# Optimization experiments

Measured on AMD Instinct MI355X. Metric: run time of the kernel, lower is better.

Reference implementation:

```python
import jax, jax.numpy as jnp
import numpy as np

BN_EPS = 1e-5


def _get_normals(radius, nsample, xyz):
    # xyz: [B, N, 3] -> normals [B, N, 3] (eigenvector of smallest eigenvalue)
    B, N, _ = xyz.shape
    sq = jnp.sum(xyz * xyz, axis=-1)                      # [B, N]
    sqrdists = sq[:, :, None] + sq[:, None, :] - 2.0 * jnp.einsum('bnc,bmc->bnm', xyz, xyz)
    ar = jnp.arange(N, dtype=jnp.int32)
    group_idx = jnp.where(sqrdists > radius * radius, N, ar[None, None, :])  # [B, N, N]
    group_idx = jnp.sort(group_idx, axis=-1)[:, :, :nsample]                 # [B, N, ns]
    group_idx = jnp.where(group_idx == N, group_idx[:, :, :1], group_idx)
    group_points = jax.vmap(lambda pts, idx: pts[idx])(xyz, group_idx)       # [B, N, ns, 3]
    centered = group_points - group_points.mean(axis=2, keepdims=True)
    cov = jnp.einsum('bnsc,bnsd->bncd', centered, centered)                  # [B, N, 3, 3]
    _, eigen_vectors = jnp.linalg.eigh(cov)
    return eigen_vectors[..., 0]


def _conv_bn(h, w, b, g, be, m, v, relu=True):
    # h: [B, N, Cin]; 1x1 Conv1d == per-point linear; BN in eval mode
    h = h @ w.T + b
    h = (h - m) / jnp.sqrt(v + BN_EPS) * g + be
    return jax.nn.relu(h) if relu else h


def setup_inputs() -> dict:
    key = jax.random.key(0)
    ks = jax.random.split(key, 32)
    B, N = 4, 4096
    inp = {
        'x': jax.random.uniform(ks[0], (B, N, 3), dtype=jnp.float32),
        'small': 0.2,
        'large': 0.3,
    }
    chans = [(1, 16), (16, 32), (32, 16), (16, 1)]
    for li, (cin, cout) in enumerate(chans, start=1):
        k = 4 * li
        inp[f'w{li}'] = jax.random.normal(ks[k], (cout, cin), dtype=jnp.float32) * (1.0 / np.sqrt(cin))
        inp[f'b{li}'] = jax.random.normal(ks[k + 1], (cout,), dtype=jnp.float32) * 0.1
        inp[f'g{li}'] = jax.random.uniform(ks[k + 2], (cout,), dtype=jnp.float32) + 0.5
        inp[f'be{li}'] = jax.random.normal(ks[k + 3], (cout,), dtype=jnp.float32) * 0.1
        inp[f'm{li}'] = jnp.zeros((cout,), dtype=jnp.float32)
        inp[f'v{li}'] = jnp.ones((cout,), dtype=jnp.float32)
    return inp


def reference(x, small, large,
              w1, b1, g1, be1, m1, v1,
              w2, b2, g2, be2, m2, v2,
              w3, b3, g3, be3, m3, v3,
              w4, b4, g4, be4, m4, v4):
    xyz = x[:, :, :3]
    small_n = _get_normals(small, 32, xyz)   # [B, N, 3]
    large_n = _get_normals(large, 64, xyz)
    curvature = jnp.linalg.norm((small_n - large_n) * 0.5, axis=2)  # [B, N]
    h = curvature[..., None]                                        # [B, N, 1]
    h = _conv_bn(h, w1, b1, g1, be1, m1, v1)
    h = _conv_bn(h, w2, b2, g2, be2, m2, v2)
    h = _conv_bn(h, w3, b3, g3, be3, m3, v3)
    h = _conv_bn(h, w4, b4, g4, be4, m4, v4, relu=False)
    return h[..., 0]                                                # [B, N]
```

## Files before the change

### kernel.cpp

```cpp
#include <hip/hip_runtime.h>
#include <math.h>

#define BLAS_FMA 1
#define SYR2_VARIANT 0

#define DEV static __device__ __forceinline__

DEV float fA(float a, float b){ return __fadd_rn(a,b); }
DEV float fSb(float a, float b){ return __fsub_rn(a,b); }
DEV float fM(float a, float b){ return __fmul_rn(a,b); }
DEV float fDv(float a, float b){ return __fdiv_rn(a,b); }
DEV float fQ(float a){ return __fsqrt_rn(a); }
DEV float fF(float a, float b, float c){ return __builtin_fmaf(a,b,c); }
DEV float fSGN(float a, float b){ return copysignf(a,b); }

DEV float slapy2f(float x, float y){
  float xa=fabsf(x), ya=fabsf(y);
  float w=fmaxf(xa,ya), z=fminf(xa,ya);
  if (z==0.0f) return w;
  float t=fDv(z,w);
  return fM(w, fQ(fA(1.0f, fM(t,t))));
}

DEV void slartgf(float f, float g, float* c, float* s, float* r){
  const float safmin=1.17549435e-38f;
  const float safmax=8.50705917e+37f;
  const float rtmin=1.08420217e-19f;
  const float rtmax=6.52169543e+18f;
  float f1=fabsf(f), g1=fabsf(g);
  if (g==0.0f){ *c=1.0f; *s=0.0f; *r=f; }
  else if (f==0.0f){ *c=0.0f; *s=fSGN(1.0f,g); *r=g1; }
  else {
    if (f1>rtmin && f1<rtmax && g1>rtmin && g1<rtmax){
      float d=fQ(fA(fM(f,f), fM(g,g)));
      *c=fDv(f1,d);
      *r=fSGN(d,f);
      *s=fDv(g,*r);
    } else {
      float u=fminf(safmax, fmaxf(safmin, fmaxf(f1,g1)));
      float fs=fDv(f,u), gs=fDv(g,u);
      float d=fQ(fA(fM(fs,fs), fM(gs,gs)));
      *c=fDv(fabsf(fs), d);
      *r=fSGN(d,f);
      *s=fDv(gs,*r);
      *r=fM(*r,u);
    }
  }
}

DEV void slaev2f(float a, float b, float c, float* rt1, float* rt2, float* cs1, float* sn1){
  float sm=fA(a,c);
  float df=fSb(a,c);
  float adf=fabsf(df);
  float tb=fA(b,b);
  float ab=fabsf(tb);
  float acmx, acmn;
  if (fabsf(a)>fabsf(c)){ acmx=a; acmn=c; } else { acmx=c; acmn=a; }
  float rt;
  if (adf>ab){ float t=fDv(ab,adf); rt=fM(adf, fQ(fA(1.0f, fM(t,t)))); }
  else if (adf<ab){ float t=fDv(adf,ab); rt=fM(ab, fQ(fA(1.0f, fM(t,t)))); }
  else { rt=fM(ab, fQ(2.0f)); }
  int sgn1;
  if (sm<0.0f){
    *rt1=fM(0.5f, fSb(sm,rt)); sgn1=-1;
    *rt2=fSb(fM(fDv(acmx,*rt1),acmn), fM(fDv(b,*rt1),b));
  } else if (sm>0.0f){
    *rt1=fM(0.5f, fA(sm,rt)); sgn1=1;
    *rt2=fSb(fM(fDv(acmx,*rt1),acmn), fM(fDv(b,*rt1),b));
  } else {
    *rt1=fM(0.5f,rt); *rt2=fM(-0.5f,rt); sgn1=1;
  }
  float cs; int sgn2;
  if (df>=0.0f){ cs=fA(df,rt); sgn2=1; } else { cs=fSb(df,rt); sgn2=-1; }
  float acs=fabsf(cs);
  if (acs>ab){
    float ct=fDv(-tb,cs);
    *sn1=fDv(1.0f, fQ(fA(1.0f, fM(ct,ct))));
    *cs1=fM(ct,*sn1);
  } else {
    if (ab==0.0f){ *cs1=1.0f; *sn1=0.0f; }
    else {
      float tn=fDv(-cs,tb);
      *cs1=fDv(1.0f, fQ(fA(1.0f, fM(tn,tn))));
      *sn1=fM(tn,*cs1);
    }
  }
  if (sgn1==sgn2){ float tn=*cs1; *cs1=-(*sn1); *sn1=tn; }
}

DEV void eig3_smallest(float a00, float a10, float a20, float a11, float a21, float a22,
                       float* vout){
  const float RMIN=3.13916472e-16f;
  const float RMAX=3.18559313e+15f;
  float anrm=fmaxf(fabsf(a00), fmaxf(fabsf(a10), fmaxf(fabsf(a20),
             fmaxf(fabsf(a11), fmaxf(fabsf(a21), fabsf(a22))))));
  if (anrm>0.0f && anrm<RMIN){
    float sig=fDv(RMIN,anrm);
    a00=fM(a00,sig); a10=fM(a10,sig); a20=fM(a20,sig);
    a11=fM(a11,sig); a21=fM(a21,sig); a22=fM(a22,sig);
  } else if (anrm>RMAX){
    float sig=fDv(RMAX,anrm);
    a00=fM(a00,sig); a10=fM(a10,sig); a20=fM(a20,sig);
    a11=fM(a11,sig); a21=fM(a21,sig); a22=fM(a22,sig);
  }
  float d0,d1,d2, e0,e1;
  float tau1=0.0f, hv2=0.0f;
  {
    float xnorm=fabsf(a20);
    if (xnorm==0.0f){
      tau1=0.0f;
      d0=a00; d1=a11; d2=a22;
      e0=a10; e1=a21;
    } else {
      float alpha=a10;
      float beta=-fSGN(slapy2f(alpha,xnorm), alpha);
      tau1=fDv(fSb(beta,alpha), beta);
      float rs=fDv(1.0f, fSb(alpha,beta));
      hv2=fM(a20, rs);
      float t2a=fM(a21, hv2);
#if BLAS_FMA
      float w1=fF(tau1, t2a, fM(tau1, a11));
      float w2=fF(fM(tau1,hv2), a22, fM(tau1, a21));
      float sd=fF(hv2, w2, w1);
#else
      float w1=fA(fM(tau1,a11), fM(tau1,t2a));
      float w2=fA(fM(tau1,a21), fM(fM(tau1,hv2),a22));
      float sd=fA(w1, fM(w2,hv2));
#endif
      float al2=fM(fM(-0.5f,tau1), sd);
      float nw1=fA(w1, al2);
#if BLAS_FMA
      float nw2=fF(al2, hv2, w2);
#else
      float nw2=fA(w2, fM(al2,hv2));
#endif
      w1=nw1; w2=nw2;
      float b11, b21, b22;
#if SYR2_VARIANT==0
      b11=fA(a11, fM(-2.0f, w1));
      b21=fA(a21, fF(hv2, -w1, -w2));
      b22=fA(a22, fF(hv2, -w2, fM(w2, -hv2)));
#elif SYR2_VARIANT==1
      b11=fSb(fSb(a11, w1), w1);
      b21=fSb(fF(hv2, -w1, a21), w2);
      b22=fF(w2, -hv2, fF(hv2, -w2, a22));
#else
      b11=fA(fA(a11, -w1), -w1);
      b21=fA(fA(a21, fM(hv2,-w1)), -w2);
      b22=fA(fA(a22, fM(hv2,-w2)), fM(w2,-hv2));
#endif
      d0=a00; d1=b11; d2=b22;
      e0=beta; e1=b21;
    }
  }
  float z0=1.0f,z1=0.0f,z2=0.0f, z3=0.0f,z4=1.0f,z5=0.0f, z6=0.0f,z7=0.0f,z8=1.0f;

#define DGET(iA)   ((iA)==0?d0:((iA)==1?d1:d2))
#define DSET(iA,vA) do{ float _dsv=(vA); int _dsi=(iA); \
  d0=(_dsi==0)?_dsv:d0; d1=(_dsi==1)?_dsv:d1; d2=(_dsi==2)?_dsv:d2; }while(0)
#define EGET(iA)   ((iA)==0?e0:e1)
#define ESET(iA,vA) do{ float _esv=(vA); int _esi=(iA); \
  e0=(_esi==0)?_esv:e0; e1=(_esi==1)?_esv:e1; }while(0)
#define ZGET(rA,cA) ((cA)==0? ((rA)==0?z0:((rA)==1?z1:z2)) : ((cA)==1? ((rA)==0?z3:((rA)==1?z4:z5)) : ((rA)==0?z6:((rA)==1?z7:z8))))
#define ZSET(rA,cA,vA) do{ float _zsv=(vA); int _zsr=(rA), _zsc=(cA); \
  z0=(_zsr==0&&_zsc==0)?_zsv:z0; z1=(_zsr==1&&_zsc==0)?_zsv:z1; z2=(_zsr==2&&_zsc==0)?_zsv:z2; \
  z3=(_zsr==0&&_zsc==1)?_zsv:z3; z4=(_zsr==1&&_zsc==1)?_zsv:z4; z5=(_zsr==2&&_zsc==1)?_zsv:z5; \
  z6=(_zsr==0&&_zsc==2)?_zsv:z6; z7=(_zsr==1&&_zsc==2)?_zsv:z7; z8=(_zsr==2&&_zsc==2)?_zsv:z8; }while(0)
#define ZROT0(ccA,ssA) do{ float _zc=(ccA), _zs=(ssA); \
  float _t0=z3, _a0=z0; z3=fSb(fM(_zc,_t0),fM(_zs,_a0)); z0=fA(fM(_zs,_t0),fM(_zc,_a0)); \
  float _t1=z4, _a1=z1; z4=fSb(fM(_zc,_t1),fM(_zs,_a1)); z1=fA(fM(_zs,_t1),fM(_zc,_a1)); \
  float _t2=z5, _a2=z2; z5=fSb(fM(_zc,_t2),fM(_zs,_a2)); z2=fA(fM(_zs,_t2),fM(_zc,_a2)); }while(0)
#define ZROT1(ccA,ssA) do{ float _zc=(ccA), _zs=(ssA); \
  float _t0=z6, _a0=z3; z6=fSb(fM(_zc,_t0),fM(_zs,_a0)); z3=fA(fM(_zs,_t0),fM(_zc,_a0)); \
  float _t1=z7, _a1=z4; z7=fSb(fM(_zc,_t1),fM(_zs,_a1)); z4=fA(fM(_zs,_t1),fM(_zc,_a1)); \
  float _t2=z8, _a2=z5; z8=fSb(fM(_zc,_t2),fM(_zs,_a2)); z5=fA(fM(_zs,_t2),fM(_zc,_a2)); }while(0)
#define ZSWAPC(caA,cbA) do{ int _zwa=(caA), _zwb=(cbA); \
  _Pragma("unroll") \
  for (int _zwr=0;_zwr<3;++_zwr){ \
    float _zwta=ZGET(_zwr,_zwa); float _zwtb=ZGET(_zwr,_zwb); \
    ZSET(_zwr,_zwa,_zwtb); ZSET(_zwr,_zwb,_zwta); \
  } }while(0)

  const float EPS=5.96046448e-08f;
  const float EPS2=3.55271368e-15f;
  const float SAFMIN=1.17549435e-38f;
  const float SSFMAX=3.07445735e+18f;
  const float SSFMIN=3.05175781e-05f;
  int l1=1, jtot=0; const int nmaxit=90;
  bool skip_sort=false;
  while (l1<=3){
    if (l1>1) ESET(l1-2, 0.0f);
    int m=3;
    for (int mm=l1; mm<=2; ++mm){
      float tst=fabsf(EGET(mm-1));
      if (tst==0.0f){ m=mm; break; }
      if (tst<=fM(fM(fQ(fabsf(DGET(mm-1))), fQ(fabsf(DGET(mm)))), EPS)){ ESET(mm-1,0.0f); m=mm; break; }
    }
    int l=l1, lsv=l, lend=m, lendsv=m;
    l1=m+1;
    if (lend==l) continue;
    float anorm=fabsf(DGET(lend-1));
    for (int i=l; i<=lend-1; ++i){ anorm=fmaxf(anorm,fabsf(DGET(i-1))); anorm=fmaxf(anorm,fabsf(EGET(i-1))); }
    if (anorm==0.0f) continue;
    int iscale=0;
    if (anorm>SSFMAX){
      iscale=1; float mv=fDv(SSFMAX,anorm);
      for (int i=l;i<=lend;++i) DSET(i-1, fM(DGET(i-1),mv));
      for (int i=l;i<=lend-1;++i) ESET(i-1, fM(EGET(i-1),mv));
    } else if (anorm<SSFMIN){
      iscale=2; float mv=fDv(SSFMIN,anorm);
      for (int i=l;i<=lend;++i) DSET(i-1, fM(DGET(i-1),mv));
      for (int i=l;i<=lend-1;++i) ESET(i-1, fM(EGET(i-1),mv));
    }
    if (fabsf(DGET(lend-1))<fabsf(DGET(l-1))){ lend=lsv; l=lendsv; }
    if (lend>l){
      for (;;){
        int M=lend;
        if (l!=lend){
          for (int mm=l; mm<=lend-1; ++mm){
            float ee=fabsf(EGET(mm-1));
            float tst=fM(ee,ee);
            if (tst<=fA(fM(fM(EPS2,fabsf(DGET(mm-1))), fabsf(DGET(mm))), SAFMIN)){ M=mm; break; }
          }
        }
        if (M<lend) ESET(M-1,0.0f);
        float p=DGET(l-1);
        if (M==l){
          l+=1;
          if (l<=lend) continue; else break;
        }
        if (M==l+1){
          float rt1,rt2,cc,ss;
          if (l==1){
            slaev2f(d0, e0, d1, &rt1,&rt2,&cc,&ss);
            ZROT0(cc, ss);
            d0=rt1; d1=rt2; e0=0.0f;
          } else {
            slaev2f(d1, e1, d2, &rt1,&rt2,&cc,&ss);
            ZROT1(cc, ss);
            d1=rt1; d2=rt2; e1=0.0f;
          }
          l+=2;
          if (l<=lend) continue; else break;
        }
        if (jtot==nmaxit) break;
        ++jtot;
        float g=fDv(fSb(d1,p), fM(2.0f,e0));
        float r=slapy2f(g,1.0f);
        g=fA(fSb(d2,p), fDv(e0, fA(g, fSGN(r,g))));
        float s=1.0f, c=1.0f; p=0.0f;
        float cr0,cr1,sr0,sr1;
        {
          float f=fM(s,e1);
          float bb=fM(c,e1);
          slartgf(g,f,&c,&s,&r);
          g=fSb(d2,p);
          r=fA(fM(fSb(d1,g),s), fM(fM(2.0f,c),bb));
          p=fM(s,r);
          d2=fA(g,p);
          g=fSb(fM(c,r),bb);
          cr1=c; sr1=-s;
        }
        {
          float f=fM(s,e0);
          float bb=fM(c,e0);
          slartgf(g,f,&c,&s,&r);
          e1=r;
          g=fSb(d1,p);
          r=fA(fM(fSb(d0,g),s), fM(fM(2.0f,c),bb));
          p=fM(s,r);
          d1=fA(g,p);
          g=fSb(fM(c,r),bb);
          cr0=c; sr0=-s;
        }
        if (cr1!=1.0f || sr1!=0.0f) ZROT1(cr1, sr1);
        if (cr0!=1.0f || sr0!=0.0f) ZROT0(cr0, sr0);
        d0=fSb(d0,p);
        e0=g;
      }
    } else {
      for (;;){
        int M=lend;
        if (l!=lend){
          for (int mm=l; mm>=lend+1; --mm){
            float ee=fabsf(EGET(mm-2));
            float tst=fM(ee,ee);
            if (tst<=fA(fM(fM(EPS2,fabsf(DGET(mm-1))), fabsf(DGET(mm-2))), SAFMIN)){ M=mm; break; }
          }
        }
        if (M>lend) ESET(M-2,0.0f);
        float p=DGET(l-1);
        if (M==l){
          l-=1;
          if (l>=lend) continue; else break;
        }
        if (M==l-1){
          float rt1,rt2,cc,ss;
          if (l==3){
            slaev2f(d1, e1, d2, &rt1,&rt2,&cc,&ss);
            ZROT1(cc, ss);
            d1=rt1; d2=rt2; e1=0.0f;
          } else {
            slaev2f(d0, e0, d1, &rt1,&rt2,&cc,&ss);
            ZROT0(cc, ss);
            d0=rt1; d1=rt2; e0=0.0f;
          }
          l-=2;
          if (l>=lend) continue; else break;
        }
        if (jtot==nmaxit) break;
        ++jtot;
        float g=fDv(fSb(d1,p), fM(2.0f,e1));
        float r=slapy2f(g,1.0f);
        g=fA(fSb(d0,p), fDv(e1, fA(g, fSGN(r,g))));
        float s=1.0f, c=1.0f; p=0.0f;
        float cr0,cr1,sr0,sr1;
        {
          float f=fM(s,e0);
          float bb=fM(c,e0);
          slartgf(g,f,&c,&s,&r);
          g=fSb(d0,p);
          r=fA(fM(fSb(d1,g),s), fM(fM(2.0f,c),bb));
          p=fM(s,r);
          d0=fA(g,p);
          g=fSb(fM(c,r),bb);
          cr0=c; sr0=s;
        }
        {
          float f=fM(s,e1);
          float bb=fM(c,e1);
          slartgf(g,f,&c,&s,&r);
          e0=r;
          g=fSb(d1,p);
          r=fA(fM(fSb(d2,g),s), fM(fM(2.0f,c),bb));
          p=fM(s,r);
          d1=fA(g,p);
          g=fSb(fM(c,r),bb);
          cr1=c; sr1=s;
        }
        if (cr0!=1.0f || sr0!=0.0f) ZROT0(cr0, sr0);
        if (cr1!=1.0f || sr1!=0.0f) ZROT1(cr1, sr1);
        d2=fSb(d2,p);
        e1=g;
      }
    }
    if (iscale==1){
      float mv=fDv(anorm,SSFMAX);
      for (int i=lsv;i<=lendsv;++i) DSET(i-1, fM(DGET(i-1),mv));
      for (int i=lsv;i<=lendsv-1;++i) ESET(i-1, fM(EGET(i-1),mv));
    } else if (iscale==2){
      float mv=fDv(anorm,SSFMIN);
      for (int i=lsv;i<=lendsv;++i) DSET(i-1, fM(DGET(i-1),mv));
      for (int i=lsv;i<=lendsv-1;++i) ESET(i-1, fM(EGET(i-1),mv));
    }
    if (jtot>=nmaxit){ skip_sort=true; break; }
  }
  if (!skip_sort){
    for (int ii=2; ii<=3; ++ii){
      int i=ii-1, k=i; float p=DGET(i-1);
      for (int j=ii; j<=3; ++j) if (DGET(j-1)<p){ k=j; p=DGET(j-1); }
      if (k!=i){
        DSET(k-1, DGET(i-1)); DSET(i-1, p);
        ZSWAPC(i-1, k-1);
      }
    }
  }
  float o0=z0, o1=z1, o2=z2;
  if (tau1!=0.0f){
#if BLAS_FMA
    float wv=fF(hv2, o2, o1);
    float t2=fM(-tau1, wv);
    o1=fA(o1, t2);
    o2=fF(t2, hv2, o2);
#else
    float wv=fA(o1, fM(o2,hv2));
    float t2=fM(-tau1, wv);
    o1=fA(o1, t2);
    o2=fA(o2, fM(hv2,t2));
#endif
  }
  vout[0]=o0; vout[1]=o1; vout[2]=o2;
#undef DGET
#undef DSET
#undef EGET
#undef ESET
#undef ZGET
#undef ZSET
#undef ZROT0
#undef ZROT1
#undef ZSWAPC
}

struct KP {
  const float* x; const float* rs; const float* rl;
  const float *w1,*b1,*g1,*be1,*m1,*v1;
  const float *w2,*b2,*g2,*be2,*m2,*v2;
  const float *w3,*b3,*g3,*be3,*m3,*v3;
  const float *w4,*b4,*g4,*be4,*m4,*v4;
  float* out;
};

#define WS_STRIDE 128

__global__ __launch_bounds__(256) void soa_kernel(const float* __restrict__ x,
                                                  float* __restrict__ xs, float* __restrict__ ys,
                                                  float* __restrict__ zs, float* __restrict__ sq,
                                                  int BN){
  int i=blockIdx.x*256+threadIdx.x;
  if (i<BN){
    float a=x[3*i], b=x[3*i+1], c=x[3*i+2];
    xs[i]=a; ys[i]=b; zs[i]=c;
    sq[i]=fA(fA(fM(a,a),fM(b,b)),fM(c,c));
  }
}

__global__ __launch_bounds__(64) void scan_kernel(const float* __restrict__ rsp,
                                                  const float* __restrict__ rlp,
                                                  unsigned short* __restrict__ ws,
                                                  const float* __restrict__ xs,
                                                  const float* __restrict__ ys,
                                                  const float* __restrict__ zs,
                                                  const float* __restrict__ sq){
  const int lane=threadIdx.x;
  const int pt=blockIdx.x;
  const int b=pt>>12, n=pt&4095;
  const int g0=b<<12;
  const double rds=rint((double)rsp[0]*1e7)/1e7;
  const double rdl=rint((double)rlp[0]*1e7)/1e7;
  const float rr_s=(float)(rds*rds);
  const float rr_l=(float)(rdl*rdl);
  const float px=xs[g0+n], py=ys[g0+n], pz=zs[g0+n];
  const float sqn=sq[g0+n];
  unsigned short* w=ws+(size_t)pt*WS_STRIDE;
  int cs=0, cl=0;
  for (int c=0;c<64;++c){
    int j=c*64+lane;
    int gj=g0+j;
    float qx=xs[gj], qy=ys[gj], qz=zs[gj];
    float sqj=sq[gj];
    float dot=fA(fA(fM(px,qx),fM(py,qy)),fM(pz,qz));
    float d2=fSb(fA(sqn,sqj), fM(2.0f,dot));
    bool pl=!(d2>rr_l);
    bool ps=!(d2>rr_s);
    unsigned long long bl=__ballot(pl);
    unsigned long long bs=__ballot(ps);
    unsigned long long ltm=(1ull<<lane)-1ull;
    int posl=cl+__popcll(bl&ltm);
    int poss=cs+__popcll(bs&ltm);
    if (pl&&posl<64) w[posl]=(unsigned short)j;
    if (ps&&poss<32) w[64+poss]=(unsigned short)j;
    cl+=__popcll(bl); if(cl>64) cl=64;
    cs+=__popcll(bs); if(cs>32) cs=32;
    if (cs>=32&&cl>=64) break;
  }
  if (lane==0){ w[96]=(unsigned short)cl; w[97]=(unsigned short)cs; }
}

__global__ __launch_bounds__(64) void momeig_kernel(KP kp,
                                                    const unsigned short* __restrict__ ws){
  const int lane=threadIdx.x;
  if (lane>=16) return;
  const int t=blockIdx.x*16+lane;
  const int p=t>>1, which=t&1;
  const int b=p>>12;
  const float* P=kp.x+(size_t)b*(4096*3);
  const unsigned char* recB=(const unsigned char*)(ws+(size_t)p*WS_STRIDE);
  const uint4* q=(const uint4*)(recB + (which? 0 : 128));
  uint4 v0=q[0], v1=q[1], v2=q[2], v3=q[3];
  uint4 v4=q[4], v5=q[5], v6=q[6], v7=q[7];
  const unsigned int cw=*(const unsigned int*)(recB+192);
  const int cnt = which? (int)(cw&0xFFFFu) : (int)(cw>>16);
  const int trip= which? 64 : 32;
  unsigned int a[32]={v0.x,v0.y,v0.z,v0.w, v1.x,v1.y,v1.z,v1.w,
                      v2.x,v2.y,v2.z,v2.w, v3.x,v3.y,v3.z,v3.w,
                      v4.x,v4.y,v4.z,v4.w, v5.x,v5.y,v5.z,v5.w,
                      v6.x,v6.y,v6.z,v6.w, v7.x,v7.y,v7.z,v7.w};
  const int j0=(int)(a[0]&0xFFFFu);

  float sx=0.0f, sy=0.0f, sz=0.0f;
#pragma unroll
  for (int k=0;k<64;++k){
    int raw=(k&1)? (int)(a[k>>1]>>16) : (int)(a[k>>1]&0xFFFFu);
    int idx=(k<cnt)? raw : j0;
    float cx=P[3*idx], cy=P[3*idx+1], cz=P[3*idx+2];
    float nx=fA(sx,cx), ny=fA(sy,cy), nz=fA(sz,cz);
    bool en=(k<trip);
    sx=en?nx:sx; sy=en?ny:sy; sz=en?nz:sz;
  }
  const float dv=which? 64.0f : 32.0f;
  const float mx=fDv(sx,dv), my=fDv(sy,dv), mz=fDv(sz,dv);

  float c0=0,c1=0,c2=0,c3=0,c4=0,c5=0;
#pragma unroll
  for (int k=0;k<64;++k){
    int raw=(k&1)? (int)(a[k>>1]>>16) : (int)(a[k>>1]&0xFFFFu);
    int idx=(k<cnt)? raw : j0;
    float cx=fSb(P[3*idx],mx), cy=fSb(P[3*idx+1],my), cz=fSb(P[3*idx+2],mz);
    float t0=fA(c0,fM(cx,cx)), t1=fA(c1,fM(cy,cx)), t2=fA(c2,fM(cz,cx));
    float t3=fA(c3,fM(cy,cy)), t4=fA(c4,fM(cz,cy)), t5=fA(c5,fM(cz,cz));
    bool en=(k<trip);
    c0=en?t0:c0; c1=en?t1:c1; c2=en?t2:c2;
    c3=en?t3:c3; c4=en?t4:c4; c5=en?t5:c5;
  }

  float v[3];
  eig3_smallest(c0,c1,c2,c3,c4,c5,v);

  float pn0=__shfl_xor(v[0],1);
  float pn1=__shfl_xor(v[1],1);
  float pn2=__shfl_xor(v[2],1);

  if ((lane&1)==0){
    float dx=fM(fSb(v[0],pn0),0.5f);
    float dy=fM(fSb(v[1],pn1),0.5f);
    float dz=fM(fSb(v[2],pn2),0.5f);
    float curv=fQ(fA(fA(fM(dx,dx),fM(dy,dy)),fM(dz,dz)));

    float h1[16];
#pragma unroll
    for (int j=0;j<16;++j){
      float a0=fA(fM(kp.w1[j],curv), kp.b1[j]);
      a0=fA(fM(fDv(fSb(a0,kp.m1[j]), fQ(fA(kp.v1[j],1e-5f))), kp.g1[j]), kp.be1[j]);
      h1[j]=fmaxf(a0,0.0f);
    }
    float h2[32];
#pragma unroll
    for (int j=0;j<32;++j){
      float a0=0.0f;
#pragma unroll
      for (int k=0;k<16;++k) a0=fF(h1[k], kp.w2[j*16+k], a0);
      a0=fA(a0, kp.b2[j]);
      a0=fA(fM(fDv(fSb(a0,kp.m2[j]), fQ(fA(kp.v2[j],1e-5f))), kp.g2[j]), kp.be2[j]);
      h2[j]=fmaxf(a0,0.0f);
    }
    float h3[16];
#pragma unroll
    for (int j=0;j<16;++j){
      float a0=0.0f;
#pragma unroll
      for (int k=0;k<32;++k) a0=fF(h2[k], kp.w3[j*32+k], a0);
      a0=fA(a0, kp.b3[j]);
      a0=fA(fM(fDv(fSb(a0,kp.m3[j]), fQ(fA(kp.v3[j],1e-5f))), kp.g3[j]), kp.be3[j]);
      h3[j]=fmaxf(a0,0.0f);
    }
    float o=0.0f;
#pragma unroll
    for (int k=0;k<16;++k) o=fF(h3[k], kp.w4[k], o);
    o=fA(o, kp.b4[0]);
    o=fA(fM(fDv(fSb(o,kp.m4[0]), fQ(fA(kp.v4[0],1e-5f))), kp.g4[0]), kp.be4[0]);
    kp.out[p]=o;
  }
}

__global__ __launch_bounds__(256) void freq_kernel(KP kp){
  __shared__ float sP[4096*3];
  __shared__ float sSq[4096];
  __shared__ unsigned short sIdxL[64][66];
  __shared__ unsigned short sIdxS[64][34];
  __shared__ unsigned char sCntL[64], sCntS[64];
  const int tid=threadIdx.x;
  const int lane=tid&63, wid=tid>>6;
  const int b=blockIdx.x>>6;
  const int n0=(blockIdx.x&63)*64;
  const float* P=kp.x+(size_t)b*(4096*3);
  for (int i=tid;i<4096*3;i+=256) sP[i]=P[i];
  for (int j=tid;j<4096;j+=256){
    float qx=P[3*j],qy=P[3*j+1],qz=P[3*j+2];
    sSq[j]=fA(fA(fM(qx,qx),fM(qy,qy)),fM(qz,qz));
  }
  __syncthreads();
  const double rds=rint((double)kp.rs[0]*1e7)/1e7;
  const double rdl=rint((double)kp.rl[0]*1e7)/1e7;
  const float rr_s=(float)(rds*rds);
  const float rr_l=(float)(rdl*rdl);
  for (int pi=0; pi<16; ++pi){
    const int pl_i=wid*16+pi;
    const int n=n0+pl_i;
    const float px=sP[3*n], py=sP[3*n+1], pz=sP[3*n+2];
    const float sqn=sSq[n];
    int cs=0, cl=0;
    for (int c=0;c<64;++c){
      int j=c*64+lane;
      float dot=fA(fA(fM(px,sP[3*j]),fM(py,sP[3*j+1])),fM(pz,sP[3*j+2]));
      float d2=fSb(fA(sqn,sSq[j]), fM(2.0f,dot));
      bool pl_=!(d2>rr_l);
      bool ps_=!(d2>rr_s);
      unsigned long long bl=__ballot(pl_);
      unsigned long long bs=__ballot(ps_);
      unsigned long long ltm=(1ull<<lane)-1ull;
      int posl=cl+__popcll(bl&ltm);
      int poss=cs+__popcll(bs&ltm);
      if (pl_&&posl<64) sIdxL[pl_i][posl]=(unsigned short)j;
      if (ps_&&poss<32) sIdxS[pl_i][poss]=(unsigned short)j;
      cl+=__popcll(bl); if(cl>64) cl=64;
      cs+=__popcll(bs); if(cs>32) cs=32;
      if (cs>=32&&cl>=64) break;
    }
    if (lane==0){ sCntL[pl_i]=(unsigned char)cl; sCntS[pl_i]=(unsigned char)cs; }
  }
  __syncthreads();
  if (lane<16){
    const int pl_i=wid*16+lane;
    const int ptg=blockIdx.x*64+pl_i;
    const int csn=sCntS[pl_i], cln=sCntL[pl_i];
    const int j0s=sIdxS[pl_i][0], j0l=sIdxL[pl_i][0];
    float ssx=0.0f,ssy=0.0f,ssz=0.0f, slx=0.0f,sly=0.0f,slz=0.0f;
    for (int k=0;k<32;++k){
      int idx=(k<csn)?(int)sIdxS[pl_i][k]:j0s;
      ssx=fA(ssx,sP[3*idx]); ssy=fA(ssy,sP[3*idx+1]); ssz=fA(ssz,sP[3*idx+2]);
    }
    for (int k=0;k<64;++k){
      int idx=(k<cln)?(int)sIdxL[pl_i][k]:j0l;
      slx=fA(slx,sP[3*idx]); sly=fA(sly,sP[3*idx+1]); slz=fA(slz,sP[3*idx+2]);
    }
    const float msx=fDv(ssx,32.0f), msy=fDv(ssy,32.0f), msz=fDv(ssz,32.0f);
    const float mlx=fDv(slx,64.0f), mly=fDv(sly,64.0f), mlz=fDv(slz,64.0f);
    float sc0=0,sc1=0,sc2=0,sc3=0,sc4=0,sc5=0;
    for (int k=0;k<32;++k){
      int idx=(k<csn)?(int)sIdxS[pl_i][k]:j0s;
      float cx=fSb(sP[3*idx],msx), cy=fSb(sP[3*idx+1],msy), cz=fSb(sP[3*idx+2],msz);
      sc0=fA(sc0,fM(cx,cx)); sc1=fA(sc1,fM(cy,cx)); sc2=fA(sc2,fM(cz,cx));
      sc3=fA(sc3,fM(cy,cy)); sc4=fA(sc4,fM(cz,cy)); sc5=fA(sc5,fM(cz,cz));
    }
    float lc0=0,lc1=0,lc2=0,lc3=0,lc4=0,lc5=0;
    for (int k=0;k<64;++k){
      int idx=(k<cln)?(int)sIdxL[pl_i][k]:j0l;
      float cx=fSb(sP[3*idx],mlx), cy=fSb(sP[3*idx+1],mly), cz=fSb(sP[3*idx+2],mlz);
      lc0=fA(lc0,fM(cx,cx)); lc1=fA(lc1,fM(cy,cx)); lc2=fA(lc2,fM(cz,cx));
      lc3=fA(lc3,fM(cy,cy)); lc4=fA(lc4,fM(cz,cy)); lc5=fA(lc5,fM(cz,cz));
    }
    float snv[3], lnv[3];
    eig3_smallest(sc0,sc1,sc2,sc3,sc4,sc5, snv);
    eig3_smallest(lc0,lc1,lc2,lc3,lc4,lc5, lnv);
    float dx=fM(fSb(snv[0],lnv[0]),0.5f);
    float dy=fM(fSb(snv[1],lnv[1]),0.5f);
    float dz=fM(fSb(snv[2],lnv[2]),0.5f);
    float curv=fQ(fA(fA(fM(dx,dx),fM(dy,dy)),fM(dz,dz)));
    float h1[16];
#pragma unroll
    for (int j=0;j<16;++j){
      float a0=fA(fM(kp.w1[j],curv), kp.b1[j]);
      a0=fA(fM(fDv(fSb(a0,kp.m1[j]), fQ(fA(kp.v1[j],1e-5f))), kp.g1[j]), kp.be1[j]);
      h1[j]=fmaxf(a0,0.0f);
    }
    float h2[32];
#pragma unroll
    for (int j=0;j<32;++j){
      float a0=0.0f;
#pragma unroll
      for (int k=0;k<16;++k) a0=fF(h1[k], kp.w2[j*16+k], a0);
      a0=fA(a0, kp.b2[j]);
      a0=fA(fM(fDv(fSb(a0,kp.m2[j]), fQ(fA(kp.v2[j],1e-5f))), kp.g2[j]), kp.be2[j]);
      h2[j]=fmaxf(a0,0.0f);
    }
    float h3[16];
#pragma unroll
    for (int j=0;j<16;++j){
      float a0=0.0f;
#pragma unroll
      for (int k=0;k<32;++k) a0=fF(h2[k], kp.w3[j*32+k], a0);
      a0=fA(a0, kp.b3[j]);
      a0=fA(fM(fDv(fSb(a0,kp.m3[j]), fQ(fA(kp.v3[j],1e-5f))), kp.g3[j]), kp.be3[j]);
      h3[j]=fmaxf(a0,0.0f);
    }
    float o=0.0f;
#pragma unroll
    for (int k=0;k<16;++k) o=fF(h3[k], kp.w4[k], o);
    o=fA(o, kp.b4[0]);
    o=fA(fM(fDv(fSb(o,kp.m4[0]), fQ(fA(kp.v4[0],1e-5f))), kp.g4[0]), kp.be4[0]);
    kp.out[ptg]=o;
  }
}

extern "C" void kernel_launch(void* const* d_in, const int* in_sizes, int n_in,
                              void* d_out, int out_size, void* d_ws, size_t ws_size,
                              hipStream_t stream){
  (void)n_in; (void)out_size;
  KP kp;
  kp.x  =(const float*)d_in[0];
  kp.rs =(const float*)d_in[1];
  kp.rl =(const float*)d_in[2];
  kp.w1 =(const float*)d_in[3];  kp.b1 =(const float*)d_in[4];  kp.g1 =(const float*)d_in[5];
  kp.be1=(const float*)d_in[6];  kp.m1 =(const float*)d_in[7];  kp.v1 =(const float*)d_in[8];
  kp.w2 =(const float*)d_in[9];  kp.b2 =(const float*)d_in[10]; kp.g2 =(const float*)d_in[11];
  kp.be2=(const float*)d_in[12]; kp.m2 =(const float*)d_in[13]; kp.v2 =(const float*)d_in[14];
  kp.w3 =(const float*)d_in[15]; kp.b3 =(const float*)d_in[16]; kp.g3 =(const float*)d_in[17];
  kp.be3=(const float*)d_in[18]; kp.m3 =(const float*)d_in[19]; kp.v3 =(const float*)d_in[20];
  kp.w4 =(const float*)d_in[21]; kp.b4 =(const float*)d_in[22]; kp.g4 =(const float*)d_in[23];
  kp.be4=(const float*)d_in[24]; kp.m4 =(const float*)d_in[25]; kp.v4 =(const float*)d_in[26];
  kp.out=(float*)d_out;
  const int BN=in_sizes[0]/3;
  const size_t recBytes=(size_t)BN*256;
  const size_t ws_need=recBytes+(size_t)BN*16;
  if (ws_size>=ws_need){
    unsigned short* wsA=(unsigned short*)d_ws;
    float* xs=(float*)((char*)d_ws+recBytes);
    float* ys=xs+BN;
    float* zs=ys+BN;
    float* sqv=zs+BN;
    soa_kernel<<<(BN+255)/256, 256, 0, stream>>>(kp.x, xs, ys, zs, sqv, BN);
    scan_kernel<<<BN, 64, 0, stream>>>(kp.rs, kp.rl, wsA, xs, ys, zs, sqv);
    momeig_kernel<<<BN/8, 64, 0, stream>>>(kp, wsA);
  } else {
    freq_kernel<<<BN/64, 256, 0, stream>>>(kp);
  }
}
```

Baseline: 193.3 us.

## Split moment accumulation and eigen/MLP into separate kernels for full wave occupancy

The combined moments+eigen+MLP kernel used only 16 of 64 lanes per wave. It is now split in two. The moment kernel uses all 64 lanes, computing one (point, radius) covariance per lane, and writes the six covariance terms to a workspace buffer. A second kernel runs the eigen solve with two lanes per task and passes normals through shared memory to 16 lanes that run the MLP. This aims to raise lane utilisation in the gather-heavy moment pass, at the cost of an extra launch, a global round-trip for covariances, and some redundant eigen computation.

```diff
diff --git a/kernel.cpp b/kernel.cpp
--- a/kernel.cpp
+++ b/kernel.cpp
@@ -456,14 +456,14 @@
   if (lane==0){ w[96]=(unsigned short)cl; w[97]=(unsigned short)cs; }
 }
 
-__global__ __launch_bounds__(64) void momeig_kernel(KP kp,
-                                                    const unsigned short* __restrict__ ws){
+__global__ __launch_bounds__(64) void moments2_kernel(const float* __restrict__ x,
+                                                      const unsigned short* __restrict__ ws,
+                                                      float* __restrict__ covB){
   const int lane=threadIdx.x;
-  if (lane>=16) return;
-  const int t=blockIdx.x*16+lane;
+  const int t=blockIdx.x*64+lane;
   const int p=t>>1, which=t&1;
   const int b=p>>12;
-  const float* P=kp.x+(size_t)b*(4096*3);
+  const float* P=x+(size_t)b*(4096*3);
   const unsigned char* recB=(const unsigned char*)(ws+(size_t)p*WS_STRIDE);
   const uint4* q=(const uint4*)(recB + (which? 0 : 128));
   uint4 v0=q[0], v1=q[1], v2=q[2], v3=q[3];
@@ -503,17 +503,29 @@
     c3=en?t3:c3; c4=en?t4:c4; c5=en?t5:c5;
   }
 
+  float* cb=covB+(size_t)p*12+which*6;
+  cb[0]=c0; cb[1]=c1; cb[2]=c2; cb[3]=c3; cb[4]=c4; cb[5]=c5;
+}
+
+__global__ __launch_bounds__(64) void eigmlp_kernel(KP kp, const float* __restrict__ covB){
+  __shared__ float sN[32][3];
+  const int lane=threadIdx.x;
+  const int g=lane>>1;
+  const int t=blockIdx.x*32+g;
+  const int p=t>>1, which=t&1;
+  const float* cb=covB+(size_t)p*12+which*6;
   float v[3];
-  eig3_smallest(c0,c1,c2,c3,c4,c5,v);
-
-  float pn0=__shfl_xor(v[0],1);
-  float pn1=__shfl_xor(v[1],1);
-  float pn2=__shfl_xor(v[2],1);
-
-  if ((lane&1)==0){
-    float dx=fM(fSb(v[0],pn0),0.5f);
-    float dy=fM(fSb(v[1],pn1),0.5f);
-    float dz=fM(fSb(v[2],pn2),0.5f);
+  eig3_smallest(cb[0],cb[1],cb[2],cb[3],cb[4],cb[5],v);
+  if ((lane&1)==0){ sN[g][0]=v[0]; sN[g][1]=v[1]; sN[g][2]=v[2]; }
+  __syncthreads();
+
+  if (lane<16){
+    const int pt=blockIdx.x*16+lane;
+    const float* sn=sN[2*lane];
+    const float* ln=sN[2*lane+1];
+    float dx=fM(fSb(sn[0],ln[0]),0.5f);
+    float dy=fM(fSb(sn[1],ln[1]),0.5f);
+    float dz=fM(fSb(sn[2],ln[2]),0.5f);
     float curv=fQ(fA(fA(fM(dx,dx),fM(dy,dy)),fM(dz,dz)));
 
     float h1[16];
@@ -548,7 +560,7 @@
     for (int k=0;k<16;++k) o=fF(h3[k], kp.w4[k], o);
     o=fA(o, kp.b4[0]);
     o=fA(fM(fDv(fSb(o,kp.m4[0]), fQ(fA(kp.v4[0],1e-5f))), kp.g4[0]), kp.be4[0]);
-    kp.out[p]=o;
+    kp.out[pt]=o;
   }
 }
 
@@ -691,16 +703,19 @@
   kp.out=(float*)d_out;
   const int BN=in_sizes[0]/3;
   const size_t recBytes=(size_t)BN*256;
-  const size_t ws_need=recBytes+(size_t)BN*16;
+  const size_t covBytes=(size_t)BN*48;
+  const size_t ws_need=recBytes+covBytes+(size_t)BN*16;
   if (ws_size>=ws_need){
     unsigned short* wsA=(unsigned short*)d_ws;
-    float* xs=(float*)((char*)d_ws+recBytes);
+    float* covB=(float*)((char*)d_ws+recBytes);
+    float* xs=(float*)((char*)d_ws+recBytes+covBytes);
     float* ys=xs+BN;
     float* zs=ys+BN;
     float* sqv=zs+BN;
     soa_kernel<<<(BN+255)/256, 256, 0, stream>>>(kp.x, xs, ys, zs, sqv, BN);
     scan_kernel<<<BN, 64, 0, stream>>>(kp.rs, kp.rl, wsA, xs, ys, zs, sqv);
-    momeig_kernel<<<BN/8, 64, 0, stream>>>(kp, wsA);
+    moments2_kernel<<<BN/32, 64, 0, stream>>>(kp.x, wsA, covB);
+    eigmlp_kernel<<<BN/16, 64, 0, stream>>>(kp, covB);
   } else {
     freq_kernel<<<BN/64, 256, 0, stream>>>(kp);
   }
```

After: 173.4 us. 1.11x faster.
